# Kernel optimization log

Hardware: AMD Instinct MI355X
Metric: run time of the kernel (lower is better)

Reference implementation:

```python
import jax, jax.numpy as jnp
import numpy as np

INPUT_SIZE = 32
HIDDEN = 512
LAYERS = 2
B, T = 16, 2048


def _lstm_layer(x, w_ih, w_hh, b_ih, b_hh):
    """Single LSTM layer, batch_first. x: [B,T,I]. Gate order (PyTorch): i,f,g,o."""
    Bsz = x.shape[0]
    H = w_hh.shape[1]
    # Precompute input contribution for all timesteps: [B,T,4H]
    gx = jnp.einsum('bti,gi->btg', x, w_ih) + b_ih

    def step(carry, gx_t):
        h, c = carry
        g = gx_t + h @ w_hh.T + b_hh  # [B,4H]
        i, f, gg, o = jnp.split(g, 4, axis=-1)
        i = jax.nn.sigmoid(i)
        f = jax.nn.sigmoid(f)
        gg = jnp.tanh(gg)
        o = jax.nn.sigmoid(o)
        c = f * c + i * gg
        h = o * jnp.tanh(c)
        return (h, c), h

    h0 = jnp.zeros((Bsz, H), x.dtype)
    (hT, cT), hs = jax.lax.scan(step, (h0, h0), jnp.swapaxes(gx, 0, 1))
    return jnp.swapaxes(hs, 0, 1), hT, cT  # [B,T,H], [B,H], [B,H]


def setup_inputs() -> dict:
    key = jax.random.key(0)
    ks = jax.random.split(key, 11)
    s = 1.0 / np.sqrt(HIDDEN)  # PyTorch uniform init scale
    u = lambda k, shape: jax.random.uniform(k, shape, jnp.float32, -s, s)
    return {
        'x': jax.random.normal(ks[0], (B, T, INPUT_SIZE), jnp.float32),
        'w_ih0': u(ks[1], (4 * HIDDEN, INPUT_SIZE)),
        'w_hh0': u(ks[2], (4 * HIDDEN, HIDDEN)),
        'b_ih0': u(ks[3], (4 * HIDDEN,)),
        'b_hh0': u(ks[4], (4 * HIDDEN,)),
        'w_ih1': u(ks[5], (4 * HIDDEN, HIDDEN)),
        'w_hh1': u(ks[6], (4 * HIDDEN, HIDDEN)),
        'b_ih1': u(ks[7], (4 * HIDDEN,)),
        'b_hh1': u(ks[8], (4 * HIDDEN,)),
        'w_out': u(ks[9], (INPUT_SIZE, HIDDEN)),
        'b_out': u(ks[10], (INPUT_SIZE,)),
    }


def reference(x, w_ih0, w_hh0, b_ih0, b_hh0, w_ih1, w_hh1, b_ih1, b_hh1, w_out, b_out):
    h1, hT0, cT0 = _lstm_layer(x, w_ih0, w_hh0, b_ih0, b_hh0)
    h2, hT1, cT1 = _lstm_layer(h1, w_ih1, w_hh1, b_ih1, b_hh1)
    y = jnp.einsum('bth,oh->bto', h2, w_out) + b_out  # [B,T,input_size]
    h_n = jnp.stack([hT0, hT1], axis=0)  # [layers, B, H]
    c_n = jnp.stack([cT0, cT1], axis=0)
    return y, h_n, c_n
```

## Files before the change

kernel.cpp:

```cpp
#include <hip/hip_runtime.h>

#define TT   2048
#define NB   16
#define HH   512
#define NSL  32
#define HSL  16
#define KW   128
#define Y_SZ (NB*TT*32)
#define RING 256
#define RM   255

typedef __attribute__((ext_vector_type(8))) short bf16x8;
typedef __attribute__((ext_vector_type(4))) float f32x4;
typedef __attribute__((ext_vector_type(4))) unsigned u32x4;
typedef unsigned long long ull;

#define OFF_XCCV 0u
#define OFF_MODE 256u
#define OFF_PROG 512u
#define OFF_F1L  4096u
#define FLB      (4u*RING*32u*4u)
#define OFF_F1X  (OFF_F1L + FLB)
#define OFF_F2L  (OFF_F1X + FLB)
#define OFF_F2X  (OFF_F2L + FLB)
#define OFF_ZEND (OFF_F2X + FLB)
#define RSLOT    ((size_t)NB*HH)
#define RB       ((size_t)RING*RSLOT*2)
#define OFF_H1LH ((size_t)(1u<<20))
#define OFF_H1LL (OFF_H1LH + RB)
#define OFF_H1XH (OFF_H1LL + RB)
#define OFF_H1XL (OFF_H1XH + RB)
#define OFF_H2LH (OFF_H1XL + RB)
#define OFF_H2LL (OFF_H2LH + RB)
#define OFF_H2XH (OFF_H2LL + RB)
#define OFF_H2XL (OFF_H2XH + RB)
#define FB       ((size_t)TT*RSLOT*2)
#define OFF_H2FH (OFF_H2XL + RB)
#define OFF_H2FL (OFF_H2FH + FB)
#define WS_NEED  (OFF_H2FL + FB)

__device__ __forceinline__ unsigned short f2bf(float x){
  unsigned u = __float_as_uint(x);
  return (unsigned short)((u + 0x7FFFu + ((u >> 16) & 1u)) >> 16);
}
__device__ __forceinline__ float bf2f(unsigned short b){
  return __uint_as_float(((unsigned)b) << 16);
}
__device__ __forceinline__ float sigm(float v){ return 1.0f / (1.0f + __expf(-v)); }
__device__ __forceinline__ float tanh_f(float v){
  float a = fabsf(v);
  float e = __expf(-2.0f * a);
  float t = (1.0f - e) / (1.0f + e);
  return v < 0.0f ? -t : t;
}
__device__ __forceinline__ void split8(const float* __restrict__ p, bf16x8& hi, bf16x8& lo){
#pragma unroll
  for (int j = 0; j < 8; ++j){
    float w = p[j];
    unsigned short h = f2bf(w);
    hi[j] = (short)h;
    lo[j] = (short)f2bf(w - bf2f(h));
  }
}
__device__ __forceinline__ bf16x8 mk(ull a, ull b){
  union { ull u[2]; bf16x8 v; } r; r.u[0] = a; r.u[1] = b; return r.v;
}
__device__ __forceinline__ bf16x8 asfrag(u32x4 v){
  union { u32x4 u; bf16x8 b; } r; r.u = v; return r.b;
}
__device__ __forceinline__ ull ld64_lic(const ull* p){
  return __hip_atomic_load(p, __ATOMIC_RELAXED, __HIP_MEMORY_SCOPE_AGENT);
}
__device__ __forceinline__ unsigned ld32_lic(const unsigned* p){
  return __hip_atomic_load(p, __ATOMIC_RELAXED, __HIP_MEMORY_SCOPE_AGENT);
}
__device__ __forceinline__ void st64_lic(ull* p, ull v){
  __hip_atomic_store(p, v, __ATOMIC_RELAXED, __HIP_MEMORY_SCOPE_AGENT);
}
__device__ __forceinline__ void st32_lic(unsigned* p, unsigned v){
  __hip_atomic_store(p, v, __ATOMIC_RELAXED, __HIP_MEMORY_SCOPE_AGENT);
}
__device__ __forceinline__ bf16x8 ld_frag_lic(const unsigned short* p){
  return mk(ld64_lic((const ull*)p), ld64_lic((const ull*)p + 1));
}
__device__ __forceinline__ unsigned ld32_l2(const unsigned* p){
  unsigned r;
  asm volatile("buffer_inv sc0\n\t"
               "global_load_dword %0, %1, off\n\t"
               "s_waitcnt vmcnt(0)"
               : "=&v"(r) : "v"(p) : "memory");
  return r;
}
__device__ __forceinline__ void ld8_l2(const void* ph, const void* pl, u32x4* r){
  asm volatile(
    "buffer_inv sc0\n\t"
    "global_load_dwordx4 %0, %8, off\n\t"
    "global_load_dwordx4 %1, %8, off offset:64\n\t"
    "global_load_dwordx4 %2, %8, off offset:128\n\t"
    "global_load_dwordx4 %3, %8, off offset:192\n\t"
    "global_load_dwordx4 %4, %9, off\n\t"
    "global_load_dwordx4 %5, %9, off offset:64\n\t"
    "global_load_dwordx4 %6, %9, off offset:128\n\t"
    "global_load_dwordx4 %7, %9, off offset:192\n\t"
    "s_waitcnt vmcnt(0)"
    : "=&v"(r[0]),"=&v"(r[1]),"=&v"(r[2]),"=&v"(r[3]),
      "=&v"(r[4]),"=&v"(r[5]),"=&v"(r[6]),"=&v"(r[7])
    : "v"(ph), "v"(pl) : "memory");
}
__device__ __forceinline__ void st64_pl(void* p, ull v){
  asm volatile("global_store_dwordx2 %0, %1, off" :: "v"(p), "v"(v) : "memory");
}
__device__ __forceinline__ void st32_pl(unsigned* p, unsigned v){
  asm volatile("global_store_dword %0, %1, off" :: "v"(p), "v"(v) : "memory");
}

__device__ __forceinline__ int wait_hy(const unsigned* bL, const unsigned* bX,
                                       unsigned expect, int lane, int lmode, long& bud){
  if (!lmode){
    bool ok = (lane >= 32);
    while (__ballot(!ok) != 0ULL){
      if (!ok) ok = (ld32_lic(bX + lane) == expect);
      if (--bud < 0) return 0;
    }
    return 0;
  }
  bool okL = (lane >= 32);
  int k = 0;
  while (true){
    if (__ballot(!okL) == 0ULL) return 1;
    if (!okL) okL = (ld32_l2(bL + lane) == expect);
    if ((++k & 15) == 0){
      bool okX = (lane >= 32);
      if (!okX) okX = (ld32_lic(bX + lane) == expect);
      if (__ballot(!okX) == 0ULL){
        if (!okL) okL = (ld32_l2(bL + lane) == expect);
        return (__ballot(!okL) == 0ULL) ? 1 : 0;
      }
    }
    if (--bud < 0) return 0;
  }
}

__global__ __launch_bounds__(256, 1) void lstm_persist(
    const float* __restrict__ x,
    const float* __restrict__ w_ih0, const float* __restrict__ w_hh0,
    const float* __restrict__ b_ih0, const float* __restrict__ b_hh0,
    const float* __restrict__ w_ih1, const float* __restrict__ w_hh1,
    const float* __restrict__ b_ih1, const float* __restrict__ b_hh1,
    float* __restrict__ out, unsigned char* __restrict__ ws)
{
  unsigned* XCCV = (unsigned*)(ws + OFF_XCCV);
  unsigned* MODE = (unsigned*)(ws + OFF_MODE);
  unsigned* PROG = (unsigned*)(ws + OFF_PROG);
  unsigned* F1L  = (unsigned*)(ws + OFF_F1L);
  unsigned* F1X  = (unsigned*)(ws + OFF_F1X);
  unsigned* F2L  = (unsigned*)(ws + OFF_F2L);
  unsigned* F2X  = (unsigned*)(ws + OFF_F2X);
  unsigned short* H1Lh = (unsigned short*)(ws + OFF_H1LH);
  unsigned short* H1Ll = (unsigned short*)(ws + OFF_H1LL);
  unsigned short* H1Xh = (unsigned short*)(ws + OFF_H1XH);
  unsigned short* H1Xl = (unsigned short*)(ws + OFF_H1XL);
  unsigned short* H2Lh = (unsigned short*)(ws + OFF_H2LH);
  unsigned short* H2Ll = (unsigned short*)(ws + OFF_H2LL);
  unsigned short* H2Xh = (unsigned short*)(ws + OFF_H2XH);
  unsigned short* H2Xl = (unsigned short*)(ws + OFF_H2XL);
  unsigned short* H2Fh = (unsigned short*)(ws + OFF_H2FH);
  unsigned short* H2Fl = (unsigned short*)(ws + OFF_H2FL);

  const int tid  = threadIdx.x;
  const int lane = tid & 63;
  const int wv   = tid >> 6;
  const int m16  = lane & 15;
  const int quad = lane >> 4;

  const int bid = blockIdx.x;
  const int xs  = bid & 7;
  const int pos = bid >> 3;
  if (xs >= 2 || pos >= NSL) return;
  const int layer = xs;
  const int sl    = pos;
  const int role  = layer * NSL + sl;
  const int j0    = sl * HSL;
  const int kwb   = wv * KW;

  long bud = 3000000;

  if (tid == 0){
    unsigned xcc = 0xDEAD;
    asm volatile("s_getreg_b32 %0, hwreg(HW_REG_XCC_ID)" : "=s"(xcc));
    st32_lic(XCCV + role, (xcc & 255u) | 0x100u);
  }
  __syncthreads();
  if (bid == 0 && wv == 0){
    bool got = false; unsigned v = 0;
    long b2 = 2000000;
    while (true){
      if (!got){ v = ld32_lic(XCCV + lane); got = (v & 0x100u) != 0u; }
      if (__ballot(!got) == 0ULL) break;
      if (--b2 < 0) break;
    }
    unsigned v0  = (unsigned)__shfl((int)v, 0, 64);
    unsigned v32 = (unsigned)__shfl((int)v, 32, 64);
    bool ok = got && ((lane < 32) ? (v == v0) : (v == v32));
    unsigned mode = (__ballot(!ok) == 0ULL) ? 1u : 0u;
    if (lane == 0) st32_lic(MODE, mode | 0x100u);
  }
  __shared__ unsigned s_mode;
  if (tid == 0){
    unsigned m = 0; long b3 = 2000000;
    do { m = ld32_lic(MODE); } while (!(m & 0x100u) && --b3 > 0);
    s_mode = m;
  }
  __syncthreads();
  int lmode = ((s_mode & 0x100u) && (s_mode & 1u)) ? 1 : 0;

  const float* Wh  = layer ? w_hh1 : w_hh0;
  const float* biL = layer ? b_ih1 : b_ih0;
  const float* bhL = layer ? b_hh1 : b_hh0;

  bf16x8 Bh_hi[4][4], Bh_lo[4][4];
#pragma unroll
  for (int g = 0; g < 4; ++g)
#pragma unroll
    for (int c = 0; c < 4; ++c){
      int row = g*HH + j0 + m16;
      int k0  = kwb + c*32 + quad*8;
      split8(Wh + (size_t)row*HH + k0, Bh_hi[g][c], Bh_lo[g][c]);
    }
  bf16x8 Bi_hi[4][4], Bi_lo[4][4];
  if (layer){
#pragma unroll
    for (int g = 0; g < 4; ++g)
#pragma unroll
      for (int c = 0; c < 4; ++c){
        int row = g*HH + j0 + m16;
        int k0  = kwb + c*32 + quad*8;
        split8(w_ih1 + (size_t)row*HH + k0, Bi_hi[g][c], Bi_lo[g][c]);
      }
  } else if (wv == 0){
#pragma unroll
    for (int g = 0; g < 4; ++g){
      int row = g*HH + j0 + m16;
      split8(w_ih0 + (size_t)row*32 + quad*8, Bi_hi[g][0], Bi_lo[g][0]);
    }
  }

  const int eb = tid >> 4;
  const int ej = tid & 15;
  float bias[4];
#pragma unroll
  for (int g = 0; g < 4; ++g){
    int r = g*HH + j0 + ej;
    bias[g] = biL[r] + bhL[r];
  }

  float cst = 0.0f;
  __shared__ float P[4][4][16][16];
  unsigned minp = 0;

  for (int t = 0; t < TT; ++t){
    const unsigned srec = (unsigned)t & RM;
    const unsigned spub = (unsigned)(t+1) & RM;
    f32x4 acc[4];
#pragma unroll
    for (int g = 0; g < 4; ++g) acc[g] = f32x4{0.f, 0.f, 0.f, 0.f};

    if (layer == 0){
      if (wv == 0){
        const float* xp = x + ((size_t)m16*TT + t)*32 + quad*8;
        bf16x8 ah, al;
#pragma unroll
        for (int j = 0; j < 8; ++j){
          float v = xp[j];
          unsigned short h = f2bf(v);
          ah[j] = (short)h;
          al[j] = (short)f2bf(v - bf2f(h));
        }
#pragma unroll
        for (int g = 0; g < 4; ++g){
          acc[g] = __builtin_amdgcn_mfma_f32_16x16x32_bf16(ah, Bi_hi[g][0], acc[g], 0, 0, 0);
          acc[g] = __builtin_amdgcn_mfma_f32_16x16x32_bf16(al, Bi_hi[g][0], acc[g], 0, 0, 0);
          acc[g] = __builtin_amdgcn_mfma_f32_16x16x32_bf16(ah, Bi_lo[g][0], acc[g], 0, 0, 0);
        }
      }
      while ((long)(t+1) - (long)minp > 250L){
        unsigned v = (lane < 32) ? ld32_lic(PROG + lane) : 0xFFFFFFFFu;
        unsigned m = v;
#pragma unroll
        for (int o = 1; o < 32; o <<= 1){
          unsigned ov = (unsigned)__shfl_xor((int)m, o, 32);
          m = m < ov ? m : ov;
        }
        minp = (unsigned)__shfl((int)m, 0, 64);
        if (--bud < 0) break;
      }
      int got = lmode;
      if (t > 0){
        got = wait_hy(F1L + ((size_t)wv*RING + srec)*32,
                      F1X + ((size_t)wv*RING + srec)*32, (unsigned)t, lane, lmode, bud);
        if (!got) lmode = 0;
      }
      const size_t rb = ((size_t)srec*NB + m16)*HH + kwb + quad*8;
      u32x4 r[8];
      if (got) ld8_l2(H1Lh + rb, H1Ll + rb, r);
      else {
#pragma unroll
        for (int c = 0; c < 4; ++c){
          r[c]   = (u32x4)__builtin_bit_cast(u32x4, ld_frag_lic(H1Xh + rb + c*32));
          r[4+c] = (u32x4)__builtin_bit_cast(u32x4, ld_frag_lic(H1Xl + rb + c*32));
        }
      }
#pragma unroll
      for (int c = 0; c < 4; ++c){
        bf16x8 ah = asfrag(r[c]);
        bf16x8 al = asfrag(r[4+c]);
#pragma unroll
        for (int g = 0; g < 4; ++g){
          acc[g] = __builtin_amdgcn_mfma_f32_16x16x32_bf16(ah, Bh_hi[g][c], acc[g], 0, 0, 0);
          acc[g] = __builtin_amdgcn_mfma_f32_16x16x32_bf16(al, Bh_hi[g][c], acc[g], 0, 0, 0);
          acc[g] = __builtin_amdgcn_mfma_f32_16x16x32_bf16(ah, Bh_lo[g][c], acc[g], 0, 0, 0);
        }
      }
    } else {
      wait_hy(F1X + ((size_t)wv*RING + spub)*32,
              F1X + ((size_t)wv*RING + spub)*32, (unsigned)(t+1), lane, 0, bud);
      {
        const size_t ib = ((size_t)spub*NB + m16)*HH + kwb + quad*8;
#pragma unroll
        for (int c = 0; c < 4; ++c){
          bf16x8 ah = ld_frag_lic(H1Xh + ib + c*32);
          bf16x8 al = ld_frag_lic(H1Xl + ib + c*32);
#pragma unroll
          for (int g = 0; g < 4; ++g){
            acc[g] = __builtin_amdgcn_mfma_f32_16x16x32_bf16(ah, Bi_hi[g][c], acc[g], 0, 0, 0);
            acc[g] = __builtin_amdgcn_mfma_f32_16x16x32_bf16(al, Bi_hi[g][c], acc[g], 0, 0, 0);
            acc[g] = __builtin_amdgcn_mfma_f32_16x16x32_bf16(ah, Bi_lo[g][c], acc[g], 0, 0, 0);
          }
        }
      }
      int got = lmode;
      if (t > 0){
        got = wait_hy(F2L + ((size_t)wv*RING + srec)*32,
                      F2X + ((size_t)wv*RING + srec)*32, (unsigned)t, lane, lmode, bud);
        if (!got) lmode = 0;
      }
      const size_t rb = ((size_t)srec*NB + m16)*HH + kwb + quad*8;
      u32x4 r[8];
      if (got) ld8_l2(H2Lh + rb, H2Ll + rb, r);
      else {
#pragma unroll
        for (int c = 0; c < 4; ++c){
          r[c]   = (u32x4)__builtin_bit_cast(u32x4, ld_frag_lic(H2Xh + rb + c*32));
          r[4+c] = (u32x4)__builtin_bit_cast(u32x4, ld_frag_lic(H2Xl + rb + c*32));
        }
      }
#pragma unroll
      for (int c = 0; c < 4; ++c){
        bf16x8 ah = asfrag(r[c]);
        bf16x8 al = asfrag(r[4+c]);
#pragma unroll
        for (int g = 0; g < 4; ++g){
          acc[g] = __builtin_amdgcn_mfma_f32_16x16x32_bf16(ah, Bh_hi[g][c], acc[g], 0, 0, 0);
          acc[g] = __builtin_amdgcn_mfma_f32_16x16x32_bf16(al, Bh_hi[g][c], acc[g], 0, 0, 0);
          acc[g] = __builtin_amdgcn_mfma_f32_16x16x32_bf16(ah, Bh_lo[g][c], acc[g], 0, 0, 0);
        }
      }
    }

#pragma unroll
    for (int g = 0; g < 4; ++g)
#pragma unroll
      for (int r = 0; r < 4; ++r)
        P[wv][g][quad*4 + r][m16] = acc[g][r];
    __syncthreads();

    float G[4];
#pragma unroll
    for (int g = 0; g < 4; ++g)
      G[g] = P[0][g][eb][ej] + P[1][g][eb][ej] + P[2][g][eb][ej] + P[3][g][eb][ej] + bias[g];

    float gi = sigm(G[0]);
    float gf = sigm(G[1]);
    float gc = tanh_f(G[2]);
    float go = sigm(G[3]);
    cst = gf*cst + gi*gc;
    float h = go * tanh_f(cst);

    if (t == TT-1){
      size_t o = (size_t)layer*NB*HH + (size_t)eb*HH + (j0 + ej);
      out[Y_SZ + o] = h;
      out[Y_SZ + 2*NB*HH + o] = cst;
    }

    unsigned short hhi = f2bf(h);
    unsigned short hlo = f2bf(h - bf2f(hhi));
    ull h1s = (ull)(unsigned short)__shfl_down((int)hhi, 1, 64);
    ull h2s = (ull)(unsigned short)__shfl_down((int)hhi, 2, 64);
    ull h3s = (ull)(unsigned short)__shfl_down((int)hhi, 3, 64);
    ull l1s = (ull)(unsigned short)__shfl_down((int)hlo, 1, 64);
    ull l2s = (ull)(unsigned short)__shfl_down((int)hlo, 2, 64);
    ull l3s = (ull)(unsigned short)__shfl_down((int)hlo, 3, 64);
    if ((ej & 3) == 0){
      ull vh = (ull)hhi | (h1s << 16) | (h2s << 32) | (h3s << 48);
      ull vl = (ull)hlo | (l1s << 16) | (l2s << 32) | (l3s << 48);
      size_t pr = (((size_t)spub*NB + eb)*HH + (unsigned)(j0 + ej)) >> 2;
      if (layer == 0){
        st64_pl((ull*)H1Lh + pr, vh);
        st64_pl((ull*)H1Ll + pr, vl);
        st64_lic((ull*)H1Xh + pr, vh);
        st64_lic((ull*)H1Xl + pr, vl);
      } else {
        size_t pf = (((size_t)t*NB + eb)*HH + (unsigned)(j0 + ej)) >> 2;
        st64_pl((ull*)H2Lh + pr, vh);
        st64_pl((ull*)H2Ll + pr, vl);
        st64_pl((ull*)H2Fh + pf, vh);
        st64_pl((ull*)H2Fl + pf, vl);
        st64_lic((ull*)H2Xh + pr, vh);
        st64_lic((ull*)H2Xl + pr, vl);
      }
    }

    asm volatile("s_waitcnt vmcnt(2)" ::: "memory");
    __syncthreads();
    if (tid == 0){
      unsigned val = (unsigned)(t+1);
      unsigned* FL = layer ? F2L : F1L;
#pragma unroll
      for (int r2 = 0; r2 < 4; ++r2)
        st32_pl(FL + ((size_t)r2*RING + spub)*32 + sl, val);
    }
    asm volatile("s_waitcnt vmcnt(0)" ::: "memory");
    __syncthreads();
    if (tid == 0){
      unsigned val = (unsigned)(t+1);
      unsigned* FX = layer ? F2X : F1X;
#pragma unroll
      for (int r2 = 0; r2 < 4; ++r2)
        st32_lic(FX + ((size_t)r2*RING + spub)*32 + sl, val);
      if (layer) st32_lic(PROG + sl, val);
    }
  }
}

__global__ __launch_bounds__(256, 1) void y_proj(
    const unsigned short* __restrict__ Hhi2, const unsigned short* __restrict__ Hlo2,
    const float* __restrict__ w_out, const float* __restrict__ b_out,
    float* __restrict__ out)
{
  __shared__ float hsh[NB][HH + 1];
  __shared__ float wsh[32][HH + 1];
  const int tid = threadIdx.x;
  const int t = blockIdx.x;

  for (int i = tid; i < 32*HH; i += 256){
    int o = i >> 9, k = i & (HH-1);
    wsh[o][k] = w_out[i];
  }
  for (int i = tid; i < NB*HH; i += 256){
    int b = i >> 9, k = i & (HH-1);
    size_t off = ((size_t)t*NB + b)*HH + k;
    hsh[b][k] = bf2f(Hhi2[off]) + bf2f(Hlo2[off]);
  }
  __syncthreads();

  const int o = tid & 31, bg = tid >> 5;
  float a0 = 0.f, a1 = 0.f;
  for (int k = 0; k < HH; ++k){
    float w = wsh[o][k];
    a0 += w * hsh[bg][k];
    a1 += w * hsh[bg + 8][k];
  }
  float bo = b_out[o];
  out[((size_t)bg*TT + t)*32 + o] = a0 + bo;
  out[((size_t)(bg+8)*TT + t)*32 + o] = a1 + bo;
}

extern "C" void kernel_launch(void* const* d_in, const int* in_sizes, int n_in,
                              void* d_out, int out_size, void* d_ws, size_t ws_size,
                              hipStream_t stream)
{
  (void)in_sizes; (void)n_in; (void)out_size;
  const float* x     = (const float*)d_in[0];
  const float* w_ih0 = (const float*)d_in[1];
  const float* w_hh0 = (const float*)d_in[2];
  const float* b_ih0 = (const float*)d_in[3];
  const float* b_hh0 = (const float*)d_in[4];
  const float* w_ih1 = (const float*)d_in[5];
  const float* w_hh1 = (const float*)d_in[6];
  const float* b_ih1 = (const float*)d_in[7];
  const float* b_hh1 = (const float*)d_in[8];
  const float* w_out = (const float*)d_in[9];
  const float* b_out = (const float*)d_in[10];
  float* out = (float*)d_out;
  unsigned char* ws = (unsigned char*)d_ws;

  if (ws_size < WS_NEED) return;

  hipMemsetAsync(ws, 0, OFF_ZEND, stream);
  hipMemsetAsync(ws + OFF_H1LH, 0, RSLOT*2, stream);
  hipMemsetAsync(ws + OFF_H1LL, 0, RSLOT*2, stream);
  hipMemsetAsync(ws + OFF_H1XH, 0, RSLOT*2, stream);
  hipMemsetAsync(ws + OFF_H1XL, 0, RSLOT*2, stream);
  hipMemsetAsync(ws + OFF_H2LH, 0, RSLOT*2, stream);
  hipMemsetAsync(ws + OFF_H2LL, 0, RSLOT*2, stream);
  hipMemsetAsync(ws + OFF_H2XH, 0, RSLOT*2, stream);
  hipMemsetAsync(ws + OFF_H2XL, 0, RSLOT*2, stream);

  lstm_persist<<<dim3(512), dim3(256), 0, stream>>>(
      x, w_ih0, w_hh0, b_ih0, b_hh0, w_ih1, w_hh1, b_ih1, b_hh1, out, ws);

  const unsigned short* H2Fh = (const unsigned short*)(ws + OFF_H2FH);
  const unsigned short* H2Fl = (const unsigned short*)(ws + OFF_H2FL);
  y_proj<<<dim3(TT), dim3(256), 0, stream>>>(H2Fh, H2Fl, w_out, b_out, out);
}
```

Baseline: 10.78 ms.

## Prefetch layer-1 input projection for next step after publishing hidden state

Layer-1 blocks now compute the input-side MFMA contribution (h1 of step t+1 times W_ih1) at the end of the previous iteration, after publishing their own flags. The next step then starts directly from the recurrent wait, which moves the input wait, load and MFMAs off the serial critical path between consecutive layer-1 steps. Flag comparisons change from == to >= to tolerate counters that are already ahead, the ring-slack threshold is tightened slightly, and the 8 fragment loads are issued as one batched asm block. The risk is added register pressure from carrying accIn across iterations, and a stricter layer-0 throttle.

```diff
diff --git a/kernel.cpp b/kernel.cpp
--- a/kernel.cpp
+++ b/kernel.cpp
@@ -107,6 +107,21 @@
       "=&v"(r[4]),"=&v"(r[5]),"=&v"(r[6]),"=&v"(r[7])
     : "v"(ph), "v"(pl) : "memory");
 }
+__device__ __forceinline__ void ld8_lic(const void* ph, const void* pl, u32x4* r){
+  asm volatile(
+    "global_load_dwordx4 %0, %8, off sc0 sc1\n\t"
+    "global_load_dwordx4 %1, %8, off offset:64 sc0 sc1\n\t"
+    "global_load_dwordx4 %2, %8, off offset:128 sc0 sc1\n\t"
+    "global_load_dwordx4 %3, %8, off offset:192 sc0 sc1\n\t"
+    "global_load_dwordx4 %4, %9, off sc0 sc1\n\t"
+    "global_load_dwordx4 %5, %9, off offset:64 sc0 sc1\n\t"
+    "global_load_dwordx4 %6, %9, off offset:128 sc0 sc1\n\t"
+    "global_load_dwordx4 %7, %9, off offset:192 sc0 sc1\n\t"
+    "s_waitcnt vmcnt(0)"
+    : "=&v"(r[0]),"=&v"(r[1]),"=&v"(r[2]),"=&v"(r[3]),
+      "=&v"(r[4]),"=&v"(r[5]),"=&v"(r[6]),"=&v"(r[7])
+    : "v"(ph), "v"(pl) : "memory");
+}
 __device__ __forceinline__ void st64_pl(void* p, ull v){
   asm volatile("global_store_dwordx2 %0, %1, off" :: "v"(p), "v"(v) : "memory");
 }
@@ -119,7 +134,7 @@
   if (!lmode){
     bool ok = (lane >= 32);
     while (__ballot(!ok) != 0ULL){
-      if (!ok) ok = (ld32_lic(bX + lane) == expect);
+      if (!ok) ok = (ld32_lic(bX + lane) >= expect);
       if (--bud < 0) return 0;
     }
     return 0;
@@ -128,16 +143,23 @@
   int k = 0;
   while (true){
     if (__ballot(!okL) == 0ULL) return 1;
-    if (!okL) okL = (ld32_l2(bL + lane) == expect);
+    if (!okL) okL = (ld32_l2(bL + lane) >= expect);
     if ((++k & 15) == 0){
       bool okX = (lane >= 32);
-      if (!okX) okX = (ld32_lic(bX + lane) == expect);
+      if (!okX) okX = (ld32_lic(bX + lane) >= expect);
       if (__ballot(!okX) == 0ULL){
-        if (!okL) okL = (ld32_l2(bL + lane) == expect);
+        if (!okL) okL = (ld32_l2(bL + lane) >= expect);
         return (__ballot(!okL) == 0ULL) ? 1 : 0;
       }
     }
     if (--bud < 0) return 0;
+  }
+}
+__device__ __forceinline__ void wait_lic(const unsigned* bX, unsigned expect, int lane, long& bud){
+  bool ok = (lane >= 32);
+  while (__ballot(!ok) != 0ULL){
+    if (!ok) ok = (ld32_lic(bX + lane) >= expect);
+    if (--bud < 0) return;
   }
 }
 
@@ -258,14 +280,35 @@
   __shared__ float P[4][4][16][16];
   unsigned minp = 0;
 
+  f32x4 accIn[4];
+#pragma unroll
+  for (int g = 0; g < 4; ++g) accIn[g] = f32x4{0.f, 0.f, 0.f, 0.f};
+  if (layer){
+    wait_lic(F1X + ((size_t)wv*RING + 1)*32, 1u, lane, bud);
+    const size_t ib = ((size_t)1*NB + m16)*HH + kwb + quad*8;
+    u32x4 r[8];
+    ld8_lic(H1Xh + ib, H1Xl + ib, r);
+#pragma unroll
+    for (int c = 0; c < 4; ++c){
+      bf16x8 ah = asfrag(r[c]);
+      bf16x8 al = asfrag(r[4+c]);
+#pragma unroll
+      for (int g = 0; g < 4; ++g){
+        accIn[g] = __builtin_amdgcn_mfma_f32_16x16x32_bf16(ah, Bi_hi[g][c], accIn[g], 0, 0, 0);
+        accIn[g] = __builtin_amdgcn_mfma_f32_16x16x32_bf16(al, Bi_hi[g][c], accIn[g], 0, 0, 0);
+        accIn[g] = __builtin_amdgcn_mfma_f32_16x16x32_bf16(ah, Bi_lo[g][c], accIn[g], 0, 0, 0);
+      }
+    }
+  }
+
   for (int t = 0; t < TT; ++t){
     const unsigned srec = (unsigned)t & RM;
     const unsigned spub = (unsigned)(t+1) & RM;
     f32x4 acc[4];
-#pragma unroll
-    for (int g = 0; g < 4; ++g) acc[g] = f32x4{0.f, 0.f, 0.f, 0.f};
 
     if (layer == 0){
+#pragma unroll
+      for (int g = 0; g < 4; ++g) acc[g] = f32x4{0.f, 0.f, 0.f, 0.f};
       if (wv == 0){
         const float* xp = x + ((size_t)m16*TT + t)*32 + quad*8;
         bf16x8 ah, al;
@@ -283,7 +326,7 @@
           acc[g] = __builtin_amdgcn_mfma_f32_16x16x32_bf16(ah, Bi_lo[g][0], acc[g], 0, 0, 0);
         }
       }
-      while ((long)(t+1) - (long)minp > 250L){
+      while ((long)(t+1) - (long)minp > 248L){
         unsigned v = (lane < 32) ? ld32_lic(PROG + lane) : 0xFFFFFFFFu;
         unsigned m = v;
 #pragma unroll
@@ -322,22 +365,8 @@
         }
       }
     } else {
-      wait_hy(F1X + ((size_t)wv*RING + spub)*32,
-              F1X + ((size_t)wv*RING + spub)*32, (unsigned)(t+1), lane, 0, bud);
-      {
-        const size_t ib = ((size_t)spub*NB + m16)*HH + kwb + quad*8;
-#pragma unroll
-        for (int c = 0; c < 4; ++c){
-          bf16x8 ah = ld_frag_lic(H1Xh + ib + c*32);
-          bf16x8 al = ld_frag_lic(H1Xl + ib + c*32);
-#pragma unroll
-          for (int g = 0; g < 4; ++g){
-            acc[g] = __builtin_amdgcn_mfma_f32_16x16x32_bf16(ah, Bi_hi[g][c], acc[g], 0, 0, 0);
-            acc[g] = __builtin_amdgcn_mfma_f32_16x16x32_bf16(al, Bi_hi[g][c], acc[g], 0, 0, 0);
-            acc[g] = __builtin_amdgcn_mfma_f32_16x16x32_bf16(ah, Bi_lo[g][c], acc[g], 0, 0, 0);
-          }
-        }
-      }
+#pragma unroll
+      for (int g = 0; g < 4; ++g) acc[g] = accIn[g];
       int got = lmode;
       if (t > 0){
         got = wait_hy(F2L + ((size_t)wv*RING + srec)*32,
@@ -410,11 +439,11 @@
         st64_lic((ull*)H1Xh + pr, vh);
         st64_lic((ull*)H1Xl + pr, vl);
       } else {
-        size_t pf = (((size_t)t*NB + eb)*HH + (unsigned)(j0 + ej)) >> 2;
+        size_t pf_ = (((size_t)t*NB + eb)*HH + (unsigned)(j0 + ej)) >> 2;
         st64_pl((ull*)H2Lh + pr, vh);
         st64_pl((ull*)H2Ll + pr, vl);
-        st64_pl((ull*)H2Fh + pf, vh);
-        st64_pl((ull*)H2Fl + pf, vl);
+        st64_pl((ull*)H2Fh + pf_, vh);
+        st64_pl((ull*)H2Fl + pf_, vl);
         st64_lic((ull*)H2Xh + pr, vh);
         st64_lic((ull*)H2Xl + pr, vl);
       }
@@ -438,6 +467,27 @@
       for (int r2 = 0; r2 < 4; ++r2)
         st32_lic(FX + ((size_t)r2*RING + spub)*32 + sl, val);
       if (layer) st32_lic(PROG + sl, val);
+    }
+
+    if (layer && t + 1 < TT){
+#pragma unroll
+      for (int g = 0; g < 4; ++g) accIn[g] = f32x4{0.f, 0.f, 0.f, 0.f};
+      const unsigned nslot = (unsigned)(t+2) & RM;
+      wait_lic(F1X + ((size_t)wv*RING + nslot)*32, (unsigned)(t+2), lane, bud);
+      const size_t nb_ = ((size_t)nslot*NB + m16)*HH + kwb + quad*8;
+      u32x4 r[8];
+      ld8_lic(H1Xh + nb_, H1Xl + nb_, r);
+#pragma unroll
+      for (int c = 0; c < 4; ++c){
+        bf16x8 ah = asfrag(r[c]);
+        bf16x8 al = asfrag(r[4+c]);
+#pragma unroll
+        for (int g = 0; g < 4; ++g){
+          accIn[g] = __builtin_amdgcn_mfma_f32_16x16x32_bf16(ah, Bi_hi[g][c], accIn[g], 0, 0, 0);
+          accIn[g] = __builtin_amdgcn_mfma_f32_16x16x32_bf16(al, Bi_hi[g][c], accIn[g], 0, 0, 0);
+          accIn[g] = __builtin_amdgcn_mfma_f32_16x16x32_bf16(ah, Bi_lo[g][c], accIn[g], 0, 0, 0);
+        }
+      }
     }
   }
 }
```

New measurement: 9.687 ms. 1.11x faster.
